# Kernel optimization log

Hardware: AMD Instinct MI355X
Metric: run time of the kernel (lower is better)

Reference implementation:

```python
import jax, jax.numpy as jnp
import numpy as np

B, T, D = 8, 2048, 1024
HID, OUT, H, WIN = 1024, 512, 4, 9
GAMMA, BIAS_ = 0.6, 0.2


def _window_mask(t, win):
    idx = jnp.clip(jnp.arange(t)[:, None] - win // 2 + jnp.arange(win)[None, :], 0, t - 1)
    return jnp.zeros((t, t), jnp.float32).at[jnp.arange(t)[:, None], idx].set(1.0)


def setup_inputs() -> dict:
    key = jax.random.key(0)
    ks = jax.random.split(key, 10)
    s = lambda d: np.float32(1.0 / np.sqrt(d))
    return {
        'x': jax.random.normal(ks[0], (B, T, D), jnp.float32),
        'seq_len': jax.random.randint(ks[1], (B,), 1, T),
        'Wq': jax.random.normal(ks[2], (D, HID), jnp.float32) * s(D),
        'bq': jnp.zeros((HID,), jnp.float32),
        'Wk': jax.random.normal(ks[3], (D, HID), jnp.float32) * s(D),
        'bk': jnp.zeros((HID,), jnp.float32),
        'Wv': jax.random.normal(ks[4], (D, HID), jnp.float32) * s(D),
        'bv': jnp.zeros((HID,), jnp.float32),
        'Wo': jax.random.normal(ks[5], (HID, D), jnp.float32) * s(HID),
        'bo': jnp.zeros((D,), jnp.float32),
        'ln_g': jnp.ones((D,), jnp.float32),
        'ln_b': jnp.zeros((D,), jnp.float32),
        'W1': jax.random.normal(ks[6], (D // 2, D), jnp.float32) * s(D),   # 1x1 conv d_model -> d_model//2
        'b1': jnp.zeros((D // 2,), jnp.float32),
        'W2': jax.random.normal(ks[7], (OUT, D // 2), jnp.float32) * s(D // 2),  # 1x1 conv -> out_dim
        'b2': jnp.zeros((OUT,), jnp.float32),
        'adj_w': jnp.float32(GAMMA),
        'adj_b': jnp.float32(BIAS_),
    }


def reference(x, seq_len, Wq, bq, Wk, bk, Wv, bv, Wo, bo, ln_g, ln_b, W1, b1, W2, b2, adj_w, adj_b):
    b, t, d = x.shape
    dk = HID // H
    # DistanceAdj: exp(-|w * dist^2 - b|), dist = |i - j|  -> [T, T], broadcast over batch
    dist = jnp.abs(jnp.arange(t)[:, None] - jnp.arange(t)[None, :]).astype(jnp.float32)
    adj = jnp.exp(-jnp.abs(adj_w * dist * dist - adj_b))
    mask = _window_mask(t, WIN)
    # TCA: multi-head attention with window mask + distance-adjacency bias
    q = (x @ Wq + bq).reshape(b, t, H, dk).transpose(0, 2, 1, 3)
    k = (x @ Wk + bk).reshape(b, t, H, dk).transpose(0, 2, 1, 3)
    v = (x @ Wv + bv).reshape(b, t, H, dk).transpose(0, 2, 1, 3)
    scores = jnp.einsum('bhqd,bhkd->bhqk', q, k) / jnp.sqrt(jnp.float32(dk))
    scores = scores + adj[None, None]
    scores = jnp.where(mask[None, None] == 0.0, jnp.float32(-1e9), scores)
    attn = jax.nn.softmax(scores, axis=-1)
    o = jnp.einsum('bhqk,bhkd->bhqd', attn, v).transpose(0, 2, 1, 3).reshape(b, t, HID)
    o = o @ Wo + bo
    # residual + LayerNorm
    y = x + o
    mu = jnp.mean(y, axis=-1, keepdims=True)
    var = jnp.mean((y - mu) ** 2, axis=-1, keepdims=True)
    y = (y - mu) * jax.lax.rsqrt(var + 1e-5) * ln_g + ln_b
    yt = y.transpose(0, 2, 1)  # [B, D, T]
    # 1x1 conv FFN with exact (erf) GELU; dropout is identity in eval
    h1 = jax.nn.gelu(jnp.einsum('od,bdt->bot', W1, yt) + b1[None, :, None], approximate=False)
    xe = jax.nn.gelu(jnp.einsum('oc,bct->bot', W2, h1) + b2[None, :, None], approximate=False)
    return xe, h1
```

## Files before the change

### kernel.cpp

```cpp
#include <hip/hip_runtime.h>
#include <hip/hip_bf16.h>
#include <math.h>

#define B_    8
#define T_    2048
#define D_    1024
#define HID_  1024
#define H_    4
#define DK_   256
#define S_ELEMS ((size_t)16384 * 1024)

typedef __bf16 bf16x8  __attribute__((ext_vector_type(8)));
typedef __bf16 bf16x4v __attribute__((ext_vector_type(4)));
typedef float  f32x4   __attribute__((ext_vector_type(4)));

__device__ __forceinline__ float gelu_f(float x) {
    return 0.5f * x * (1.0f + erff(x * 0.70710678118654752440f));
}

__device__ __forceinline__ void gload_lds16(const void* g, void* s) {
    __builtin_amdgcn_global_load_lds(
        (const __attribute__((address_space(1))) void*)g,
        (__attribute__((address_space(3))) void*)s, 16, 0, 0);
}

template<int EPI>
__global__ __launch_bounds__(512) void gemm256_k(
    const __bf16* __restrict__ A, const __bf16* __restrict__ Bt,
    const float* __restrict__ bias, const float* __restrict__ res,
    float* __restrict__ Cf, __bf16* __restrict__ Cb,
    int M, int N, int K)
{
    __shared__ __bf16 lds[2][2][256 * 64];
    const int tid = threadIdx.x;
    const int w  = tid >> 6, l = tid & 63;
    const int wm = w >> 2,  wn = w & 3;
    const int lr = l & 15, lq = l >> 4, lx = l & 7;
    const int m0 = blockIdx.x * 256, n0 = blockIdx.y * 256;
    const int nt = K >> 6;

    f32x4 acc[8][4] = {};

    int srow[4], sslot[4];
    #pragma unroll
    for (int c = 0; c < 4; ++c) {
        int i = tid + c * 512;
        srow[c]  = i >> 3;
        sslot[c] = (i & 7) ^ (srow[c] & 7);
    }
    const int ldsu = (w * 64) * 16;

    auto stageA = [&](int t) {
        char* dst = (char*)&lds[t & 1][0][0];
        #pragma unroll
        for (int c = 0; c < 4; ++c)
            gload_lds16((const char*)(A + (size_t)(m0 + srow[c]) * K + t * 64) + (sslot[c] << 4),
                        dst + ldsu + c * 512 * 16);
    };
    auto stageB = [&](int t) {
        char* dst = (char*)&lds[t & 1][1][0];
        #pragma unroll
        for (int c = 0; c < 4; ++c)
            gload_lds16((const char*)(Bt + (size_t)(n0 + srow[c]) * K + t * 64) + (sslot[c] << 4),
                        dst + ldsu + c * 512 * 16);
    };

    stageA(0);
    stageB(0);

    for (int t = 0; t < nt; ++t) {
        const int cur = t & 1;
        if (t + 1 < nt) {
            stageA(t + 1);
            stageB(t + 1);
            asm volatile("s_waitcnt vmcnt(8)" ::: "memory");
        } else {
            asm volatile("s_waitcnt vmcnt(0)" ::: "memory");
        }
        __builtin_amdgcn_s_barrier();
        asm volatile("" ::: "memory");

        const char* Ap = (const char*)&lds[cur][0][0];
        const char* Bp = (const char*)&lds[cur][1][0];

        bf16x8 af[2][4], bfr[2][2][2];

        auto rdA = [&](int ah) {
            #pragma unroll
            for (int ks = 0; ks < 2; ++ks)
                #pragma unroll
                for (int fi = 0; fi < 4; ++fi)
                    af[ks][fi] = *(const bf16x8*)(Ap + (wm * 128 + (ah * 4 + fi) * 16 + lr) * 128
                                                     + ((((ks << 2) | lq) ^ lx) << 4));
        };
        auto rdB = [&](int bh) {
            #pragma unroll
            for (int ks = 0; ks < 2; ++ks)
                #pragma unroll
                for (int fj = 0; fj < 2; ++fj)
                    bfr[bh][ks][fj] = *(const bf16x8*)(Bp + (wn * 64 + (bh * 2 + fj) * 16 + lr) * 128
                                                          + ((((ks << 2) | lq) ^ lx) << 4));
        };
        auto mm = [&](int ah, int bh) {
            __builtin_amdgcn_s_setprio(1);
            #pragma unroll
            for (int ks = 0; ks < 2; ++ks)
                #pragma unroll
                for (int fi = 0; fi < 4; ++fi)
                    #pragma unroll
                    for (int fj = 0; fj < 2; ++fj)
                        acc[ah * 4 + fi][bh * 2 + fj] = __builtin_amdgcn_mfma_f32_16x16x32_bf16(
                            af[ks][fi], bfr[bh][ks][fj], acc[ah * 4 + fi][bh * 2 + fj], 0, 0, 0);
            __builtin_amdgcn_s_setprio(0);
        };

        rdA(0); rdB(0);
        mm(0, 0);
        __builtin_amdgcn_s_barrier();
        asm volatile("" ::: "memory");
        rdB(1);
        mm(0, 1);
        __builtin_amdgcn_s_barrier();
        asm volatile("" ::: "memory");
        rdA(1);
        mm(1, 1);
        __builtin_amdgcn_s_barrier();
        asm volatile("" ::: "memory");
        mm(1, 0);
        __builtin_amdgcn_s_barrier();
        asm volatile("" ::: "memory");
    }

    #pragma unroll
    for (int fi = 0; fi < 8; ++fi) {
        const int row0 = m0 + wm * 128 + fi * 16 + lq * 4;
        #pragma unroll
        for (int fj = 0; fj < 4; ++fj) {
            const int col = n0 + wn * 64 + fj * 16 + lr;
            const float bz = bias[col];
            if (EPI == 0) {
                const int sel = col >> 10, cl = col & 1023;
                __bf16* out = Cb + (size_t)sel * S_ELEMS + (size_t)row0 * 1024 + cl;
                #pragma unroll
                for (int r = 0; r < 4; ++r)
                    out[(size_t)r * 1024] = (__bf16)(acc[fi][fj][r] + bz);
            } else {
                #pragma unroll
                for (int r = 0; r < 4; ++r) {
                    size_t idx = (size_t)(row0 + r) * N + col;
                    Cb[idx] = (__bf16)(acc[fi][fj][r] + bz + res[idx]);
                }
            }
        }
    }
}

template<int EPI>
__global__ __launch_bounds__(256) void mm_k(
    const __bf16* __restrict__ A, const __bf16* __restrict__ Bt,
    const float* __restrict__ bias, const float* __restrict__ res,
    float* __restrict__ Cf, __bf16* __restrict__ Cb,
    int M, int N, int K)
{
    __shared__ __bf16 As[128 * 32];
    __shared__ __bf16 Bs[128 * 32];
    const int tid = threadIdx.x;
    const int w   = tid >> 6;
    const int l   = tid & 63;
    const int wm  = w >> 1, wn = w & 1;
    const int m0  = blockIdx.x * 128, n0 = blockIdx.y * 128;
    const int lr  = l & 15;
    const int lq  = l >> 4;

    f32x4 acc[4][4] = {};

    const int ar0 = tid >> 2,          ak0 = (tid & 3) * 8;
    const int ar1 = (tid + 256) >> 2,  ak1 = (tid & 3) * 8;
    char* As_b = (char*)As;
    char* Bs_b = (char*)Bs;
    char* ldsA0 = As_b + (w * 64) * 16;
    char* ldsA1 = As_b + (w * 64 + 256) * 16;
    char* ldsB0 = Bs_b + (w * 64) * 16;
    char* ldsB1 = Bs_b + (w * 64 + 256) * 16;

    for (int k0 = 0; k0 < K; k0 += 32) {
        gload_lds16(A  + (size_t)(m0 + ar0) * K + k0 + ak0, ldsA0);
        gload_lds16(A  + (size_t)(m0 + ar1) * K + k0 + ak1, ldsA1);
        gload_lds16(Bt + (size_t)(n0 + ar0) * K + k0 + ak0, ldsB0);
        gload_lds16(Bt + (size_t)(n0 + ar1) * K + k0 + ak1, ldsB1);
        __syncthreads();

        const __bf16* Ab = As + (wm * 64 + lr) * 32 + lq * 8;
        const __bf16* Bb = Bs + (wn * 64 + lr) * 32 + lq * 8;
        bf16x8 a[4], b[4];
        #pragma unroll
        for (int i = 0; i < 4; ++i) a[i] = *(const bf16x8*)(Ab + i * 16 * 32);
        #pragma unroll
        for (int j = 0; j < 4; ++j) b[j] = *(const bf16x8*)(Bb + j * 16 * 32);
        #pragma unroll
        for (int i = 0; i < 4; ++i)
            #pragma unroll
            for (int j = 0; j < 4; ++j)
                acc[i][j] = __builtin_amdgcn_mfma_f32_16x16x32_bf16(
                    a[i], b[j], acc[i][j], 0, 0, 0);
        __syncthreads();
    }

    #pragma unroll
    for (int i = 0; i < 4; ++i) {
        const int row0 = m0 + wm * 64 + i * 16 + lq * 4;
        #pragma unroll
        for (int j = 0; j < 4; ++j) {
            const int col = n0 + wn * 64 + j * 16 + lr;
            const float bz = bias[col];
            float gv[4];
            #pragma unroll
            for (int r = 0; r < 4; ++r) gv[r] = gelu_f(acc[i][j][r] + bz);
            const int bidx = row0 >> 11, t0 = row0 & (T_ - 1);
            float4 g4; g4.x = gv[0]; g4.y = gv[1]; g4.z = gv[2]; g4.w = gv[3];
            *(float4*)(Cf + (size_t)bidx * N * T_ + (size_t)col * T_ + t0) = g4;
            if (EPI == 2) {
                #pragma unroll
                for (int r = 0; r < 4; ++r)
                    Cb[(size_t)(row0 + r) * N + col] = (__bf16)gv[r];
            }
        }
    }
}

__global__ __launch_bounds__(256) void attn3_k(
    const __bf16* Q, const __bf16* __restrict__ Kg, const __bf16* __restrict__ Vg,
    __bf16* O, const float* __restrict__ aw_p, const float* __restrict__ ab_p)
{
    const int tid = threadIdx.x;
    const int g  = tid & 7;
    const int ql = tid >> 3;
    const int b  = blockIdx.x >> 8;
    const int h  = (blockIdx.x >> 6) & 3;
    const int t  = ((blockIdx.x & 63) << 5) + ql;

    const size_t hbase = (size_t)b * T_ * HID_ + h * DK_ + g * 32;

    const __bf16* qp = Q + hbase + (size_t)t * HID_;
    float qf[32];
    #pragma unroll
    for (int c = 0; c < 4; ++c) {
        bf16x8 v = *(const bf16x8*)(qp + c * 8);
        #pragma unroll
        for (int e = 0; e < 8; ++e) qf[c * 8 + e] = (float)v[e];
    }

    float part[9];
    #pragma unroll
    for (int jj = 0; jj < 9; ++jj) {
        int j  = t - 4 + jj;
        int jc = min(max(j, 0), T_ - 1);
        const __bf16* kp = Kg + hbase + (size_t)jc * HID_;
        float s = 0.f;
        #pragma unroll
        for (int c = 0; c < 4; ++c) {
            bf16x8 kv = *(const bf16x8*)(kp + c * 8);
            #pragma unroll
            for (int e = 0; e < 8; ++e) s = fmaf(qf[c * 8 + e], (float)kv[e], s);
        }
        part[jj] = s;
    }

    #pragma unroll
    for (int jj = 0; jj < 9; ++jj) {
        float v = part[jj];
        v += __shfl_xor(v, 1);
        v += __shfl_xor(v, 2);
        v += __shfl_xor(v, 4);
        part[jj] = v;
    }

    const float aw = *aw_p, ab = *ab_p;
    float sc[9], mx = -1e30f;
    #pragma unroll
    for (int jj = 0; jj < 9; ++jj) {
        int j = t - 4 + jj;
        float d = (float)(jj - 4);
        float adj = __expf(-fabsf(aw * d * d - ab));
        sc[jj] = (j >= 0 && j < T_) ? part[jj] * (1.0f / 16.0f) + adj : -1e30f;
        mx = fmaxf(mx, sc[jj]);
    }
    float wgt[9], sum = 0.f;
    #pragma unroll
    for (int jj = 0; jj < 9; ++jj) { wgt[jj] = __expf(sc[jj] - mx); sum += wgt[jj]; }
    const float inv = 1.0f / sum;

    float o[32];
    #pragma unroll
    for (int e = 0; e < 32; ++e) o[e] = 0.f;
    #pragma unroll
    for (int jj = 0; jj < 9; ++jj) {
        int jc = min(max(t - 4 + jj, 0), T_ - 1);
        const float wj = wgt[jj] * inv;
        const __bf16* vp = Vg + hbase + (size_t)jc * HID_;
        #pragma unroll
        for (int c = 0; c < 4; ++c) {
            bf16x8 vv = *(const bf16x8*)(vp + c * 8);
            #pragma unroll
            for (int e = 0; e < 8; ++e)
                o[c * 8 + e] = fmaf(wj, (float)vv[e], o[c * 8 + e]);
        }
    }

    __bf16* op = O + hbase + (size_t)t * HID_;
    #pragma unroll
    for (int c = 0; c < 4; ++c) {
        bf16x8 ov;
        #pragma unroll
        for (int e = 0; e < 8; ++e) ov[e] = (__bf16)o[c * 8 + e];
        *(bf16x8*)(op + c * 8) = ov;
    }
}

__device__ __forceinline__ float block_sum(float v, float* sm) {
    #pragma unroll
    for (int off = 32; off; off >>= 1) v += __shfl_xor(v, off);
    if ((threadIdx.x & 63) == 0) sm[threadIdx.x >> 6] = v;
    __syncthreads();
    float r = sm[0] + sm[1] + sm[2] + sm[3];
    __syncthreads();
    return r;
}

__global__ __launch_bounds__(256) void ln_k(
    __bf16* __restrict__ Yb, const float* __restrict__ g, const float* __restrict__ bta)
{
    __shared__ float sm[4];
    __bf16* y = Yb + (size_t)blockIdx.x * D_;
    bf16x4v v4 = *(const bf16x4v*)(y + threadIdx.x * 4);
    float v[4] = { (float)v4[0], (float)v4[1], (float)v4[2], (float)v4[3] };
    float mean = block_sum(v[0] + v[1] + v[2] + v[3], sm) * (1.0f / D_);
    float s2 = 0.f;
    #pragma unroll
    for (int i = 0; i < 4; ++i) { float d = v[i] - mean; s2 += d * d; }
    float rstd = rsqrtf(block_sum(s2, sm) * (1.0f / D_) + 1e-5f);
    bf16x4v o;
    #pragma unroll
    for (int i = 0; i < 4; ++i) {
        int idx = threadIdx.x * 4 + i;
        o[i] = (__bf16)((v[i] - mean) * rstd * g[idx] + bta[idx]);
    }
    *(bf16x4v*)(y + threadIdx.x * 4) = o;
}

__global__ __launch_bounds__(256) void prep_k(
    const float4* __restrict__ x4, const float4* __restrict__ W14,
    const float4* __restrict__ W24,
    const float* __restrict__ bq, const float* __restrict__ bk,
    const float* __restrict__ bv,
    bf16x4v* __restrict__ xb4, bf16x4v* __restrict__ W1b4,
    bf16x4v* __restrict__ W2b4, float* __restrict__ bqkvd)
{
    const int bid = blockIdx.x, tid = threadIdx.x;
    if (bid < 16384) {
        int i = bid * 256 + tid;
        float4 v = x4[i];
        bf16x4v o; o[0] = (__bf16)v.x; o[1] = (__bf16)v.y; o[2] = (__bf16)v.z; o[3] = (__bf16)v.w;
        xb4[i] = o;
    } else if (bid < 16896) {
        int i = (bid - 16384) * 256 + tid;
        float4 v = W14[i];
        bf16x4v o; o[0] = (__bf16)v.x; o[1] = (__bf16)v.y; o[2] = (__bf16)v.z; o[3] = (__bf16)v.w;
        W1b4[i] = o;
    } else if (bid < 17152) {
        int i = (bid - 16896) * 256 + tid;
        float4 v = W24[i];
        bf16x4v o; o[0] = (__bf16)v.x; o[1] = (__bf16)v.y; o[2] = (__bf16)v.z; o[3] = (__bf16)v.w;
        W2b4[i] = o;
    } else {
        int i = (bid - 17152) * 256 + tid;
        bqkvd[i] = (i < 1024) ? bq[i] : ((i < 2048) ? bk[i - 1024] : bv[i - 2048]);
    }
}

__global__ void castT4_k(const float* __restrict__ Wq, const float* __restrict__ Wk,
                         const float* __restrict__ Wv, const float* __restrict__ Wo,
                         __bf16* __restrict__ Wqkv, __bf16* __restrict__ Wot)
{
    __shared__ float tbuf[32][33];
    const int z = blockIdx.z;
    const float* in = (z == 0) ? Wq : (z == 1) ? Wk : (z == 2) ? Wv : Wo;
    __bf16* out = (z < 3) ? (Wqkv + (size_t)z * 1024 * 1024) : Wot;
    int k0 = blockIdx.x * 32, n0 = blockIdx.y * 32;
    for (int r = threadIdx.y; r < 32; r += 8)
        tbuf[r][threadIdx.x] = in[(size_t)(k0 + r) * 1024 + n0 + threadIdx.x];
    __syncthreads();
    for (int r = threadIdx.y; r < 32; r += 8)
        out[(size_t)(n0 + r) * 1024 + k0 + threadIdx.x] = (__bf16)tbuf[threadIdx.x][r];
}

extern "C" void kernel_launch(void* const* d_in, const int* in_sizes, int n_in,
                              void* d_out, int out_size, void* d_ws, size_t ws_size,
                              hipStream_t stream) {
    const float* x    = (const float*)d_in[0];
    const float* Wq   = (const float*)d_in[2];
    const float* bq   = (const float*)d_in[3];
    const float* Wk   = (const float*)d_in[4];
    const float* bk   = (const float*)d_in[5];
    const float* Wv   = (const float*)d_in[6];
    const float* bv   = (const float*)d_in[7];
    const float* Wo   = (const float*)d_in[8];
    const float* bo   = (const float*)d_in[9];
    const float* ln_g = (const float*)d_in[10];
    const float* ln_b = (const float*)d_in[11];
    const float* W1   = (const float*)d_in[12];
    const float* b1   = (const float*)d_in[13];
    const float* W2   = (const float*)d_in[14];
    const float* b2   = (const float*)d_in[15];
    const float* adj_w = (const float*)d_in[16];
    const float* adj_b = (const float*)d_in[17];

    const int M = B_ * T_;
    const size_t S = S_ELEMS;

    __bf16* Qb   = (__bf16*)d_ws;
    __bf16* Kb   = Qb + S;
    __bf16* Vb   = Kb + S;
    __bf16* Yb   = Kb;
    __bf16* xb   = Vb + S;
    __bf16* Wqkv = xb + S;
    __bf16* Wot  = Wqkv + 3 * 1024 * 1024;
    __bf16* W1b  = Wot + 1024 * 1024;
    __bf16* W2b  = W1b + 512 * 1024;
    __bf16* h1b  = W2b + 512 * 512;
    float*  bqkvd = (float*)(h1b + (size_t)M * 512);

    float* xe = (float*)d_out;
    float* h1 = xe + (size_t)B_ * 512 * T_;

    dim3 blk(256);

    prep_k<<<dim3(17164), blk, 0, stream>>>(
        (const float4*)x, (const float4*)W1, (const float4*)W2, bq, bk, bv,
        (bf16x4v*)xb, (bf16x4v*)W1b, (bf16x4v*)W2b, bqkvd);
    castT4_k<<<dim3(32, 32, 4), dim3(32, 8), 0, stream>>>(Wq, Wk, Wv, Wo, Wqkv, Wot);

    gemm256_k<0><<<dim3(M / 256, 3072 / 256), dim3(512), 0, stream>>>(
        xb, Wqkv, bqkvd, nullptr, nullptr, Qb, M, 3072, D_);

    attn3_k<<<dim3(B_ * H_ * (T_ / 32)), blk, 0, stream>>>(Qb, Kb, Vb, Qb, adj_w, adj_b);

    gemm256_k<1><<<dim3(M / 256, HID_ / 256), dim3(512), 0, stream>>>(
        Qb, Wot, bo, x, nullptr, Yb, M, D_, HID_);

    ln_k<<<dim3(M), blk, 0, stream>>>(Yb, ln_g, ln_b);

    dim3 gF(M / 128, 512 / 128);
    mm_k<2><<<gF, blk, 0, stream>>>(Yb, W1b, b1, nullptr, h1, h1b, M, 512, D_);

    mm_k<3><<<gF, blk, 0, stream>>>(h1b, W2b, b2, nullptr, xe, nullptr, M, 512, 512);
}
```

Before: 323.6 us.

## Replace FFN GEMMs with double-buffered swizzled 256x128 kernel; simplify big-GEMM inner loop

The two FFN 1x1-conv GEMMs move from a simple 128x128, K=32, single-buffered kernel to a 512-thread 256x128 tile kernel. The new kernel uses K=64 steps, XOR-swizzled LDS, and double-buffered async global-to-LDS loads overlapped with MFMA. Separately, the large 256x256 GEMM's inner loop drops its four-phase interleaved read/compute schedule with intermediate barriers in favour of a plain per-k-slice load-then-MFMA loop. This removes barriers but holds more fragments live in registers at once and gives up some LDS-read/MFMA interleaving. The FFN grid shrinks to 256 blocks, which may underfill the device.

```diff
diff --git a/kernel.cpp b/kernel.cpp
--- a/kernel.cpp
+++ b/kernel.cpp
@@ -83,50 +83,26 @@
         const char* Ap = (const char*)&lds[cur][0][0];
         const char* Bp = (const char*)&lds[cur][1][0];
 
-        bf16x8 af[2][4], bfr[2][2][2];
-
-        auto rdA = [&](int ah) {
-            #pragma unroll
-            for (int ks = 0; ks < 2; ++ks)
+        #pragma unroll
+        for (int ks = 0; ks < 2; ++ks) {
+            bf16x8 af[8], bfr[4];
+            #pragma unroll
+            for (int fi = 0; fi < 8; ++fi)
+                af[fi] = *(const bf16x8*)(Ap + (wm * 128 + fi * 16 + lr) * 128
+                                             + ((((ks << 2) | lq) ^ lx) << 4));
+            #pragma unroll
+            for (int fj = 0; fj < 4; ++fj)
+                bfr[fj] = *(const bf16x8*)(Bp + (wn * 64 + fj * 16 + lr) * 128
+                                              + ((((ks << 2) | lq) ^ lx) << 4));
+            __builtin_amdgcn_s_setprio(1);
+            #pragma unroll
+            for (int fi = 0; fi < 8; ++fi)
                 #pragma unroll
-                for (int fi = 0; fi < 4; ++fi)
-                    af[ks][fi] = *(const bf16x8*)(Ap + (wm * 128 + (ah * 4 + fi) * 16 + lr) * 128
-                                                     + ((((ks << 2) | lq) ^ lx) << 4));
-        };
-        auto rdB = [&](int bh) {
-            #pragma unroll
-            for (int ks = 0; ks < 2; ++ks)
-                #pragma unroll
-                for (int fj = 0; fj < 2; ++fj)
-                    bfr[bh][ks][fj] = *(const bf16x8*)(Bp + (wn * 64 + (bh * 2 + fj) * 16 + lr) * 128
-                                                          + ((((ks << 2) | lq) ^ lx) << 4));
-        };
-        auto mm = [&](int ah, int bh) {
-            __builtin_amdgcn_s_setprio(1);
-            #pragma unroll
-            for (int ks = 0; ks < 2; ++ks)
-                #pragma unroll
-                for (int fi = 0; fi < 4; ++fi)
-                    #pragma unroll
-                    for (int fj = 0; fj < 2; ++fj)
-                        acc[ah * 4 + fi][bh * 2 + fj] = __builtin_amdgcn_mfma_f32_16x16x32_bf16(
-                            af[ks][fi], bfr[bh][ks][fj], acc[ah * 4 + fi][bh * 2 + fj], 0, 0, 0);
+                for (int fj = 0; fj < 4; ++fj)
+                    acc[fi][fj] = __builtin_amdgcn_mfma_f32_16x16x32_bf16(
+                        af[fi], bfr[fj], acc[fi][fj], 0, 0, 0);
             __builtin_amdgcn_s_setprio(0);
-        };
-
-        rdA(0); rdB(0);
-        mm(0, 0);
-        __builtin_amdgcn_s_barrier();
-        asm volatile("" ::: "memory");
-        rdB(1);
-        mm(0, 1);
-        __builtin_amdgcn_s_barrier();
-        asm volatile("" ::: "memory");
-        rdA(1);
-        mm(1, 1);
-        __builtin_amdgcn_s_barrier();
-        asm volatile("" ::: "memory");
-        mm(1, 0);
+        }
         __builtin_amdgcn_s_barrier();
         asm volatile("" ::: "memory");
     }
@@ -156,66 +132,100 @@
 }
 
 template<int EPI>
-__global__ __launch_bounds__(256) void mm_k(
+__global__ __launch_bounds__(512) void gemmF_k(
     const __bf16* __restrict__ A, const __bf16* __restrict__ Bt,
-    const float* __restrict__ bias, const float* __restrict__ res,
+    const float* __restrict__ bias,
     float* __restrict__ Cf, __bf16* __restrict__ Cb,
     int M, int N, int K)
 {
-    __shared__ __bf16 As[128 * 32];
-    __shared__ __bf16 Bs[128 * 32];
+    __shared__ __bf16 lds[2][384 * 64];
     const int tid = threadIdx.x;
-    const int w   = tid >> 6;
-    const int l   = tid & 63;
-    const int wm  = w >> 1, wn = w & 1;
-    const int m0  = blockIdx.x * 128, n0 = blockIdx.y * 128;
-    const int lr  = l & 15;
-    const int lq  = l >> 4;
-
-    f32x4 acc[4][4] = {};
-
-    const int ar0 = tid >> 2,          ak0 = (tid & 3) * 8;
-    const int ar1 = (tid + 256) >> 2,  ak1 = (tid & 3) * 8;
-    char* As_b = (char*)As;
-    char* Bs_b = (char*)Bs;
-    char* ldsA0 = As_b + (w * 64) * 16;
-    char* ldsA1 = As_b + (w * 64 + 256) * 16;
-    char* ldsB0 = Bs_b + (w * 64) * 16;
-    char* ldsB1 = Bs_b + (w * 64 + 256) * 16;
-
-    for (int k0 = 0; k0 < K; k0 += 32) {
-        gload_lds16(A  + (size_t)(m0 + ar0) * K + k0 + ak0, ldsA0);
-        gload_lds16(A  + (size_t)(m0 + ar1) * K + k0 + ak1, ldsA1);
-        gload_lds16(Bt + (size_t)(n0 + ar0) * K + k0 + ak0, ldsB0);
-        gload_lds16(Bt + (size_t)(n0 + ar1) * K + k0 + ak1, ldsB1);
-        __syncthreads();
-
-        const __bf16* Ab = As + (wm * 64 + lr) * 32 + lq * 8;
-        const __bf16* Bb = Bs + (wn * 64 + lr) * 32 + lq * 8;
-        bf16x8 a[4], b[4];
-        #pragma unroll
-        for (int i = 0; i < 4; ++i) a[i] = *(const bf16x8*)(Ab + i * 16 * 32);
-        #pragma unroll
-        for (int j = 0; j < 4; ++j) b[j] = *(const bf16x8*)(Bb + j * 16 * 32);
-        #pragma unroll
-        for (int i = 0; i < 4; ++i)
-            #pragma unroll
-            for (int j = 0; j < 4; ++j)
-                acc[i][j] = __builtin_amdgcn_mfma_f32_16x16x32_bf16(
-                    a[i], b[j], acc[i][j], 0, 0, 0);
-        __syncthreads();
-    }
-
-    #pragma unroll
-    for (int i = 0; i < 4; ++i) {
-        const int row0 = m0 + wm * 64 + i * 16 + lq * 4;
-        #pragma unroll
-        for (int j = 0; j < 4; ++j) {
-            const int col = n0 + wn * 64 + j * 16 + lr;
+    const int w  = tid >> 6, l = tid & 63;
+    const int wm = w >> 2,  wn = w & 3;
+    const int lr = l & 15, lq = l >> 4, lx = l & 7;
+    const int m0 = blockIdx.x * 256, n0 = blockIdx.y * 128;
+    const int nt = K >> 6;
+
+    f32x4 acc[8][2] = {};
+
+    int srA[4], ssA[4], srB[2], ssB[2];
+    #pragma unroll
+    for (int c = 0; c < 4; ++c) {
+        int i = tid + c * 512;
+        srA[c] = i >> 3;
+        ssA[c] = (i & 7) ^ (srA[c] & 7);
+    }
+    #pragma unroll
+    for (int c = 0; c < 2; ++c) {
+        int i = tid + c * 512;
+        srB[c] = i >> 3;
+        ssB[c] = (i & 7) ^ (srB[c] & 7);
+    }
+    const int ldsu = (w * 64) * 16;
+
+    auto stage = [&](int t) {
+        char* dst = (char*)&lds[t & 1][0];
+        #pragma unroll
+        for (int c = 0; c < 4; ++c)
+            gload_lds16((const char*)(A + (size_t)(m0 + srA[c]) * K + t * 64) + (ssA[c] << 4),
+                        dst + ldsu + c * 512 * 16);
+        char* dstB = dst + 256 * 64 * 2;
+        #pragma unroll
+        for (int c = 0; c < 2; ++c)
+            gload_lds16((const char*)(Bt + (size_t)(n0 + srB[c]) * K + t * 64) + (ssB[c] << 4),
+                        dstB + ldsu + c * 512 * 16);
+    };
+
+    stage(0);
+
+    for (int t = 0; t < nt; ++t) {
+        const int cur = t & 1;
+        if (t + 1 < nt) {
+            stage(t + 1);
+            asm volatile("s_waitcnt vmcnt(6)" ::: "memory");
+        } else {
+            asm volatile("s_waitcnt vmcnt(0)" ::: "memory");
+        }
+        __builtin_amdgcn_s_barrier();
+        asm volatile("" ::: "memory");
+
+        const char* Ap = (const char*)&lds[cur][0];
+        const char* Bp = Ap + 256 * 64 * 2;
+
+        #pragma unroll
+        for (int ks = 0; ks < 2; ++ks) {
+            bf16x8 af[8], bfr[2];
+            #pragma unroll
+            for (int fi = 0; fi < 8; ++fi)
+                af[fi] = *(const bf16x8*)(Ap + (wm * 128 + fi * 16 + lr) * 128
+                                             + ((((ks << 2) | lq) ^ lx) << 4));
+            #pragma unroll
+            for (int fj = 0; fj < 2; ++fj)
+                bfr[fj] = *(const bf16x8*)(Bp + (wn * 32 + fj * 16 + lr) * 128
+                                              + ((((ks << 2) | lq) ^ lx) << 4));
+            __builtin_amdgcn_s_setprio(1);
+            #pragma unroll
+            for (int fi = 0; fi < 8; ++fi)
+                #pragma unroll
+                for (int fj = 0; fj < 2; ++fj)
+                    acc[fi][fj] = __builtin_amdgcn_mfma_f32_16x16x32_bf16(
+                        af[fi], bfr[fj], acc[fi][fj], 0, 0, 0);
+            __builtin_amdgcn_s_setprio(0);
+        }
+        __builtin_amdgcn_s_barrier();
+        asm volatile("" ::: "memory");
+    }
+
+    #pragma unroll
+    for (int fi = 0; fi < 8; ++fi) {
+        const int row0 = m0 + wm * 128 + fi * 16 + lq * 4;
+        #pragma unroll
+        for (int fj = 0; fj < 2; ++fj) {
+            const int col = n0 + wn * 32 + fj * 16 + lr;
             const float bz = bias[col];
             float gv[4];
             #pragma unroll
-            for (int r = 0; r < 4; ++r) gv[r] = gelu_f(acc[i][j][r] + bz);
+            for (int r = 0; r < 4; ++r) gv[r] = gelu_f(acc[fi][fj][r] + bz);
             const int bidx = row0 >> 11, t0 = row0 & (T_ - 1);
             float4 g4; g4.x = gv[0]; g4.y = gv[1]; g4.z = gv[2]; g4.w = gv[3];
             *(float4*)(Cf + (size_t)bidx * N * T_ + (size_t)col * T_ + t0) = g4;
@@ -450,8 +460,9 @@
 
     ln_k<<<dim3(M), blk, 0, stream>>>(Yb, ln_g, ln_b);
 
-    dim3 gF(M / 128, 512 / 128);
-    mm_k<2><<<gF, blk, 0, stream>>>(Yb, W1b, b1, nullptr, h1, h1b, M, 512, D_);
-
-    mm_k<3><<<gF, blk, 0, stream>>>(h1b, W2b, b2, nullptr, xe, nullptr, M, 512, 512);
-}
+    gemmF_k<2><<<dim3(M / 256, 512 / 128), dim3(512), 0, stream>>>(
+        Yb, W1b, b1, h1, h1b, M, 512, D_);
+
+    gemmF_k<3><<<dim3(M / 256, 512 / 128), dim3(512), 0, stream>>>(
+        h1b, W2b, b2, xe, nullptr, M, 512, 512);
+}
```

Result: no change. 319.2 us (-1.4%).
